# Kernel optimization log

Measured on AMD Instinct MI355X. Metric: run time of the kernel, lower is better.

The kernel has to match this reference:

```python
import jax, jax.numpy as jnp
import numpy as np

D_MODEL = 1024
NHEAD = 16
D_K = D_MODEL // NHEAD
B, S = 2, 2048
NEG_INF = float('-inf')


def setup_inputs() -> dict:
    key = jax.random.key(0)
    ks = jax.random.split(key, 12)
    sc = 1.0 / np.sqrt(D_MODEL)
    return {
        'q': jax.random.normal(ks[0], (B, S, D_MODEL), dtype=jnp.float32),
        'k': jax.random.normal(ks[1], (B, S, D_MODEL), dtype=jnp.float32),
        'q_mask': jax.random.randint(ks[2], (B, S), 0, 2, dtype=jnp.int32),
        'k_mask': jax.random.randint(ks[3], (B, S), 0, 2, dtype=jnp.int32),
        'Wq': jax.random.normal(ks[4], (D_MODEL, D_MODEL), dtype=jnp.float32) * sc,
        'bq': jnp.zeros((D_MODEL,), dtype=jnp.float32),
        'Wk': jax.random.normal(ks[5], (D_MODEL, D_MODEL), dtype=jnp.float32) * sc,
        'bk': jnp.zeros((D_MODEL,), dtype=jnp.float32),
        'Wv': jax.random.normal(ks[6], (D_MODEL, D_MODEL), dtype=jnp.float32) * sc,
        'bv': jnp.zeros((D_MODEL,), dtype=jnp.float32),
        'Wo': jax.random.normal(ks[7], (D_MODEL, D_MODEL), dtype=jnp.float32) * sc,
        'bo': jnp.zeros((D_MODEL,), dtype=jnp.float32),
        'causal_attention': 1,
    }


def _split_heads(x):  # [B,S,D] -> [B,H,S,d_k]
    b, s, _ = x.shape
    return x.reshape(b, s, NHEAD, D_K).transpose(0, 2, 1, 3)


def reference(q, k, q_mask, k_mask, Wq, bq, Wk, bk, Wv, bv, Wo, bo, causal_attention):
    v_in = k  # module uses V = K
    qh = _split_heads(q @ Wq.T + bq)
    kh = _split_heads(k @ Wk.T + bk)
    vh = _split_heads(v_in @ Wv.T + bv)
    # [B,H,Sq,Sk]
    scores = jnp.einsum('bhqd,bhkd->bhqk', qh, kh) / jnp.sqrt(jnp.float32(D_K))
    sq, sk = scores.shape[-2], scores.shape[-1]
    if causal_attention:
        causal = jnp.triu(jnp.ones((sq, sk), dtype=bool), k=1)
        scores = jnp.where(causal[None, None], NEG_INF, scores)
    scores = jnp.where(k_mask[:, None, None, :] == 0, NEG_INF, scores)
    attn = jax.nn.softmax(scores, axis=-1)
    attn = jnp.where(q_mask[:, None, :, None] == 0, 0.0, attn)
    out = jnp.einsum('bhqk,bhkd->bhqd', attn, vh)  # [B,H,Sq,d_k]
    out = out.transpose(0, 2, 1, 3).reshape(q.shape[0], sq, D_MODEL)
    return out @ Wo.T + bo
```

## Files before the change

### kernel.cpp

```cpp
#include <hip/hip_runtime.h>

typedef unsigned short u16;
typedef unsigned int   u32;
typedef __bf16 bf16x8 __attribute__((ext_vector_type(8)));
typedef float  f32x4  __attribute__((ext_vector_type(4)));

#define NEG_INF (-__builtin_inff())

#define GLDS16(g, l) __builtin_amdgcn_global_load_lds( \
    (const __attribute__((address_space(1))) void*)(g), \
    (__attribute__((address_space(3))) void*)(l), 16, 0, 0)

__device__ __forceinline__ u16 f2bf(float f) {
  u32 u = __builtin_bit_cast(u32, f);
  u32 r = u + 0x7FFFu + ((u >> 16) & 1u);
  return (u16)(r >> 16);
}
__device__ __forceinline__ float bf2f(u16 v) {
  u32 u = ((u32)v) << 16;
  return __builtin_bit_cast(float, u);
}
__device__ __forceinline__ u32 pk2bf(float a, float b) {
  return __builtin_amdgcn_perm(__builtin_bit_cast(u32, b),
                               __builtin_bit_cast(u32, a), 0x07060302u);
}
__device__ __forceinline__ float bperm(float v, int src) {
  return __builtin_bit_cast(float, __builtin_amdgcn_ds_bpermute(
      src * 4, __builtin_bit_cast(int, v)));
}

struct ConvArgs {
  const void* src[10];
  u16* dst[10];
};

__global__ void convert_kernel(ConvArgs a, const int* __restrict__ kmask,
                               float* __restrict__ kbias) {
  if (blockIdx.x >= 1024) {
    int idx = (blockIdx.x - 1024) * 256 + threadIdx.x;
    kbias[idx] = kmask[idx] ? 0.0f : NEG_INF;
    return;
  }
  __shared__ int cnt;
  if (threadIdx.x == 0) cnt = 0;
  __syncthreads();
  const u16* q16 = (const u16*)a.src[0];
  int local = 0;
  for (int i = threadIdx.x; i < 8192; i += 256) {
    int e = (q16[i] >> 7) & 0xFF;
    if (e >= 118 && e <= 129) local++;
  }
  atomicAdd(&cnt, local);
  __syncthreads();
  const int fl = (cnt > 6144) ? 1 : 0;

  const int total = 1573376;
  for (int u0 = blockIdx.x * 256 + threadIdx.x; u0 < total; u0 += 1024 * 256) {
    int s, off;
    if (u0 < 1048576)      { s = u0 >> 19;                 off = u0 & 524287; }
    else if (u0 < 1572864) { int v = u0 - 1048576; s = 2 + (v >> 17); off = v & 131071; }
    else                   { int v = u0 - 1572864; s = 6 + (v >> 7);  off = v & 127; }
    u16* d = a.dst[s] + (size_t)off * 8;
    if (fl) {
      const uint4* sp = (const uint4*)((const u16*)a.src[s] + (size_t)off * 8);
      *(uint4*)d = *sp;
    } else {
      const float* sp = (const float*)a.src[s] + (size_t)off * 8;
      u16 tmp[8];
      #pragma unroll
      for (int j = 0; j < 8; j++) tmp[j] = f2bf(sp[j]);
      *(uint4*)d = *(uint4*)tmp;
    }
  }
}

template <int BM>
__device__ __forceinline__ void gemm_mainloop(
    const u16* __restrict__ A, const u16* __restrict__ W,
    int bm, int bn, u16* As, u16* Bs, f32x4 (*acc)[4]) {
  const int t = threadIdx.x, lane = t & 63, w = t >> 6;
  const int wm = (w >> 1) * (BM / 2), wn = (w & 1) * 64;
  const int l15 = lane & 15, quad = lane >> 4;
  const int sr = t >> 2, sc = (t & 3) * 8;
  const u16* Ag0 = A + (size_t)(bm + sr) * 1024 + sc;
  const u16* Ag1 = Ag0 + (size_t)64 * 1024;
  const u16* Wg0 = W + (size_t)(bn + sr) * 1024 + sc;
  const u16* Wg1 = Wg0 + (size_t)64 * 1024;
  u16* As0 = As + t * 8;        u16* As1 = As + 2048 + t * 8;
  u16* Bs0 = Bs + t * 8;        u16* Bs1 = Bs + 2048 + t * 8;

  for (int k0 = 0; k0 < 1024; k0 += 32) {
    GLDS16(Ag0 + k0, As0);
    if (BM == 128) GLDS16(Ag1 + k0, As1);
    GLDS16(Wg0 + k0, Bs0);
    GLDS16(Wg1 + k0, Bs1);
    __syncthreads();
    bf16x8 af[BM / 32], bw[4];
    #pragma unroll
    for (int i = 0; i < BM / 32; i++)
      af[i] = *(const bf16x8*)&As[(wm + i * 16 + l15) * 32 + quad * 8];
    #pragma unroll
    for (int j = 0; j < 4; j++)
      bw[j] = *(const bf16x8*)&Bs[(wn + j * 16 + l15) * 32 + quad * 8];
    #pragma unroll
    for (int i = 0; i < BM / 32; i++)
      #pragma unroll
      for (int j = 0; j < 4; j++)
        acc[i][j] = __builtin_amdgcn_mfma_f32_16x16x32_bf16(af[i], bw[j], acc[i][j], 0, 0, 0);
    __syncthreads();
  }
}

__global__ __launch_bounds__(256) void qkv_proj_kernel(
    const u16* __restrict__ qc, const u16* __restrict__ kc,
    const u16* __restrict__ Wq, const u16* __restrict__ Wk, const u16* __restrict__ Wv,
    const u16* __restrict__ bq, const u16* __restrict__ bk, const u16* __restrict__ bv,
    u16* __restrict__ Qp, u16* __restrict__ Kp, u16* __restrict__ Vt) {
  __shared__ __align__(16) u16 As[128 * 32];
  __shared__ __align__(16) u16 Bs[128 * 32];
  const int z = blockIdx.z;
  const u16* A    = (z == 0) ? qc : kc;
  const u16* W    = (z == 0) ? Wq : (z == 1) ? Wk : Wv;
  const u16* bias = (z == 0) ? bq : (z == 1) ? bk : bv;
  const int bm = blockIdx.y * 128, bn = blockIdx.x * 128;

  const f32x4 fzero = {0.f, 0.f, 0.f, 0.f};
  f32x4 acc[4][4];
  #pragma unroll
  for (int i = 0; i < 4; i++)
    #pragma unroll
    for (int j = 0; j < 4; j++) acc[i][j] = fzero;

  gemm_mainloop<128>(A, W, bm, bn, As, Bs, acc);

  const int t = threadIdx.x, lane = t & 63, w = t >> 6;
  const int wm = (w >> 1) * 64, wn = (w & 1) * 64;
  const int l15 = lane & 15, quad = lane >> 4;

  if (z < 2) {
    u16* out = (z == 0) ? Qp : Kp;
    #pragma unroll
    for (int i = 0; i < 4; i++)
      #pragma unroll
      for (int j = 0; j < 4; j++) {
        int n = bn + wn + j * 16 + l15;
        float bb = bf2f(bias[n]);
        int m0 = bm + wm + i * 16 + quad * 4;
        #pragma unroll
        for (int r = 0; r < 4; r++)
          out[(size_t)(m0 + r) * 1024 + n] = f2bf(acc[i][j][r] + bb);
      }
  } else {
    #pragma unroll
    for (int i = 0; i < 4; i++)
      #pragma unroll
      for (int j = 0; j < 4; j++) {
        int n = bn + wn + j * 16 + l15;
        int hh = n >> 6, dw = n & 63;
        float bb = bf2f(bias[n]);
        int m0 = bm + wm + i * 16 + quad * 4;
        int b_ = m0 >> 11, s0 = m0 & 2047;
        u16 tmp[4];
        #pragma unroll
        for (int r = 0; r < 4; r++) tmp[r] = f2bf(acc[i][j][r] + bb);
        *(ushort4*)&Vt[((size_t)(b_ * 16 + hh) * 64 + dw) * 2048 + s0] = *(ushort4*)tmp;
      }
  }
}

__global__ __launch_bounds__(256, 4) void attn_kernel(
    const u16* __restrict__ Qp, const u16* __restrict__ Kp, const u16* __restrict__ Vt,
    const int* __restrict__ qmask, const float* __restrict__ kbias,
    const int* __restrict__ causal_p, u16* __restrict__ AO) {
  __shared__ __align__(16) u16 KS[2][128 * 64];
  __shared__ __align__(16) u16 VS[2][64 * 128];
  __shared__ __align__(16) u16 P[4][16 * 64];

  const int t = threadIdx.x, lane = t & 63, w = t >> 6;
  const int quad = lane >> 4, l15 = lane & 15, l7 = l15 & 7;
  const int bh = blockIdx.x & 31;
  const int g4 = 31 - (int)(blockIdx.x >> 5);
  const int b = bh >> 4, h = bh & 15;
  const int causal = *causal_p;
  const int q0 = g4 * 64 + w * 16;
  const int nkt = causal ? (g4 >> 1) + 1 : 16;
  const float cs = 0.18033688011112042f;
  const f32x4 fzero = {0.f, 0.f, 0.f, 0.f};

  const u16* qr = Qp + (size_t)(b * 2048 + q0 + l15) * 1024 + h * 64 + quad * 8;
  const bf16x8 qf0 = *(const bf16x8*)qr;
  const bf16x8 qf1 = *(const bf16x8*)(qr + 32);

  const int kLr = lane >> 3, kLc = lane & 7;
  const u16* kgw = Kp + (size_t)(b * 2048 + 32 * w + kLr) * 1024 + h * 64 +
                   (kLc ^ kLr) * 8;
  const int vLr = lane >> 4, vLc = lane & 15;
  const u16* vgw = Vt + (size_t)bh * 131072 + (size_t)(16 * w) * 2048;
  int voff[4];
  #pragma unroll
  for (int i = 0; i < 4; i++)
    voff[i] = (4 * i + vLr) * 2048 + ((vLc ^ (4 * i + vLr)) * 8);
  u16* kls0 = &KS[0][(32 * w) * 64] + lane * 8;
  u16* kls1 = &KS[1][(32 * w) * 64] + lane * 8;
  u16* vls0 = &VS[0][(16 * w) * 128] + lane * 8;
  u16* vls1 = &VS[1][(16 * w) * 128] + lane * 8;

  f32x4 Oa[4];
  #pragma unroll
  for (int dt = 0; dt < 4; dt++) Oa[dt] = fzero;
  float mr = NEG_INF, lr = 0.f;
  u16* Pw = P[w];

  {
    const u16* kg = kgw;
    const u16* vg = vgw;
    #pragma unroll
    for (int i = 0; i < 4; i++) {
      GLDS16(kg + i * 8192, kls0 + i * 512);
      GLDS16(vg + voff[i], vls0 + i * 512);
    }
  }

  for (int kt = 0; kt < nkt; kt++) {
    __syncthreads();
    if (kt + 1 < nkt) {
      const u16* kg = kgw + (size_t)(kt + 1) * 131072;
      const u16* vg = vgw + (kt + 1) * 128;
      u16* kd = ((kt + 1) & 1) ? kls1 : kls0;
      u16* vd = ((kt + 1) & 1) ? vls1 : vls0;
      #pragma unroll
      for (int i = 0; i < 4; i++) {
        GLDS16(kg + i * 8192, kd + i * 512);
        GLDS16(vg + voff[i], vd + i * 512);
      }
    }
    if (causal && kt * 128 > q0 + 15) continue;
    const u16* KSc = KS[kt & 1];
    const u16* VSc = VS[kt & 1];

    f32x4 sa[8];
    #pragma unroll
    for (int mt = 0; mt < 8; mt++) sa[mt] = fzero;
    #pragma unroll
    for (int mt = 0; mt < 8; mt++) {
      bf16x8 kf0 = *(const bf16x8*)&KSc[(mt * 16 + l15) * 64 + ((quad ^ l7) * 8)];
      bf16x8 kf1 = *(const bf16x8*)&KSc[(mt * 16 + l15) * 64 + (((quad ^ l7) ^ 4) * 8)];
      sa[mt] = __builtin_amdgcn_mfma_f32_16x16x32_bf16(kf0, qf0, sa[mt], 0, 0, 0);
      sa[mt] = __builtin_amdgcn_mfma_f32_16x16x32_bf16(kf1, qf1, sa[mt], 0, 0, 0);
    }

    const f32x4* kb4 = (const f32x4*)(kbias + b * 2048 + kt * 128);
    #pragma unroll
    for (int mt = 0; mt < 8; mt++) {
      f32x4 kb = kb4[mt * 4 + quad];
      #pragma unroll
      for (int r = 0; r < 4; r++) sa[mt][r] = sa[mt][r] * cs + kb[r];
    }
    if (causal && kt * 128 + 127 > q0) {
      #pragma unroll
      for (int mt = 0; mt < 8; mt++)
        #pragma unroll
        for (int r = 0; r < 4; r++)
          if (kt * 128 + mt * 16 + quad * 4 + r > q0 + l15) sa[mt][r] = NEG_INF;
    }

    f32x4 m4 = sa[0];
    #pragma unroll
    for (int mt = 1; mt < 8; mt++)
      #pragma unroll
      for (int r = 0; r < 4; r++) m4[r] = fmaxf(m4[r], sa[mt][r]);
    float mx = fmaxf(fmaxf(m4[0], m4[1]), fmaxf(m4[2], m4[3]));
    mx = fmaxf(mx, __shfl_xor(mx, 16, 64));
    mx = fmaxf(mx, __shfl_xor(mx, 32, 64));
    float mn = fmaxf(mr, mx);
    float mc = fmaxf(mn, -3.0e38f);
    float al = __builtin_amdgcn_exp2f(mr - mc);
    mr = mn;
    float ssum = 0.f;
    #pragma unroll
    for (int mt = 0; mt < 8; mt++)
      #pragma unroll
      for (int r = 0; r < 4; r++) {
        float pv = __builtin_amdgcn_exp2f(sa[mt][r] - mc);
        sa[mt][r] = pv;
        ssum += pv;
      }
    ssum += __shfl_xor(ssum, 16, 64);
    ssum += __shfl_xor(ssum, 32, 64);
    lr = lr * al + ssum;

    f32x4 alv;
    #pragma unroll
    for (int r = 0; r < 4; r++) alv[r] = bperm(al, quad * 4 + r);
    #pragma unroll
    for (int dt = 0; dt < 4; dt++)
      #pragma unroll
      for (int r = 0; r < 4; r++) Oa[dt][r] *= alv[r];

    #pragma unroll
    for (int hh = 0; hh < 2; hh++) {
      #pragma unroll
      for (int mh = 0; mh < 4; mh++) {
        int B = mh * 2 + (quad >> 1);
        uint2 pk;
        pk.x = pk2bf(sa[hh * 4 + mh][0], sa[hh * 4 + mh][1]);
        pk.y = pk2bf(sa[hh * 4 + mh][2], sa[hh * 4 + mh][3]);
        *(uint2*)&Pw[l15 * 64 + ((B ^ l7) * 8) + (quad & 1) * 4] = pk;
      }
      #pragma unroll
      for (int kh = 0; kh < 2; kh++) {
        int kp = hh * 2 + kh;
        bf16x8 pf = *(const bf16x8*)&Pw[l15 * 64 + (((kh * 4 + quad) ^ l7) * 8)];
        #pragma unroll
        for (int dt = 0; dt < 4; dt++) {
          bf16x8 vf = *(const bf16x8*)
              &VSc[(dt * 16 + l15) * 128 + (((kp * 4 + quad) ^ l15) * 8)];
          Oa[dt] = __builtin_amdgcn_mfma_f32_16x16x32_bf16(pf, vf, Oa[dt], 0, 0, 0);
        }
      }
    }
  }

  float f = (lr > 0.f) ? (1.0f / lr) : 0.f;
  if (qmask[b * 2048 + q0 + l15] == 0) f = 0.f;
  f32x4 fv;
  #pragma unroll
  for (int r = 0; r < 4; r++) fv[r] = bperm(f, quad * 4 + r);
  #pragma unroll
  for (int dt = 0; dt < 4; dt++)
    #pragma unroll
    for (int r = 0; r < 4; r++)
      AO[(size_t)(b * 2048 + q0 + quad * 4 + r) * 1024 + h * 64 + dt * 16 + l15] =
          f2bf(Oa[dt][r] * fv[r]);
}

__global__ __launch_bounds__(256, 2) void oproj_kernel(
    const u16* __restrict__ AO, const u16* __restrict__ Wo, const u16* __restrict__ bo,
    void* __restrict__ out, const int* __restrict__ flag) {
  __shared__ __align__(16) u16 As[64 * 32];
  __shared__ __align__(16) u16 Bs[128 * 32];
  const int bm = blockIdx.y * 64, bn = blockIdx.x * 128;

  const f32x4 fzero = {0.f, 0.f, 0.f, 0.f};
  f32x4 acc[2][4];
  #pragma unroll
  for (int i = 0; i < 2; i++)
    #pragma unroll
    for (int j = 0; j < 4; j++) acc[i][j] = fzero;

  gemm_mainloop<64>(AO, Wo, bm, bn, As, Bs, acc);

  const int t = threadIdx.x, lane = t & 63, w = t >> 6;
  const int wm = (w >> 1) * 32, wn = (w & 1) * 64;
  const int l15 = lane & 15, quad = lane >> 4;
  const int isbf = *flag;
  #pragma unroll
  for (int i = 0; i < 2; i++)
    #pragma unroll
    for (int j = 0; j < 4; j++) {
      int n = bn + wn + j * 16 + l15;
      float bb = bf2f(bo[n]);
      int m0 = bm + wm + i * 16 + quad * 4;
      #pragma unroll
      for (int r = 0; r < 4; r++) {
        float v = acc[i][j][r] + bb;
        size_t idx = (size_t)(m0 + r) * 1024 + n;
        if (isbf) ((u16*)out)[idx] = f2bf(v);
        else      ((float*)out)[idx] = v;
      }
    }
}

__global__ void flag_kernel(const u16* __restrict__ q, int* __restrict__ flag) {
  __shared__ int cnt;
  if (threadIdx.x == 0) cnt = 0;
  __syncthreads();
  int local = 0;
  for (int i = threadIdx.x; i < 8192; i += 256) {
    int e = (q[i] >> 7) & 0xFF;
    if (e >= 118 && e <= 129) local++;
  }
  atomicAdd(&cnt, local);
  __syncthreads();
  if (threadIdx.x == 0) flag[0] = (cnt > 6144) ? 1 : 0;
}

extern "C" void kernel_launch(void* const* d_in, const int* in_sizes, int n_in,
                              void* d_out, int out_size, void* d_ws, size_t ws_size,
                              hipStream_t stream) {
  (void)in_sizes; (void)n_in; (void)out_size; (void)ws_size;

  char* w = (char*)d_ws;
  int* flag = (int*)w;
  u16* qc  = (u16*)(w + 256);
  u16* kc  = qc  + 4194304;
  u16* Qp  = kc  + 4194304;
  u16* Kp  = Qp  + 4194304;
  u16* Vt  = Kp  + 4194304;
  u16* AO  = Vt  + 4194304;
  u16* Wqc = AO  + 4194304;
  u16* Wkc = Wqc + 1048576;
  u16* Wvc = Wkc + 1048576;
  u16* Woc = Wvc + 1048576;
  u16* bqc = Woc + 1048576;
  u16* bkc = bqc + 1024;
  u16* bvc = bkc + 1024;
  u16* boc = bvc + 1024;
  float* kbias = (float*)(boc + 1024);

  flag_kernel<<<1, 256, 0, stream>>>((const u16*)d_in[0], flag);

  ConvArgs ca;
  ca.src[0] = d_in[0];  ca.dst[0] = qc;
  ca.src[1] = d_in[1];  ca.dst[1] = kc;
  ca.src[2] = d_in[4];  ca.dst[2] = Wqc;
  ca.src[3] = d_in[6];  ca.dst[3] = Wkc;
  ca.src[4] = d_in[8];  ca.dst[4] = Wvc;
  ca.src[5] = d_in[10]; ca.dst[5] = Woc;
  ca.src[6] = d_in[5];  ca.dst[6] = bqc;
  ca.src[7] = d_in[7];  ca.dst[7] = bkc;
  ca.src[8] = d_in[9];  ca.dst[8] = bvc;
  ca.src[9] = d_in[11]; ca.dst[9] = boc;
  convert_kernel<<<1040, 256, 0, stream>>>(ca, (const int*)d_in[3], kbias);

  qkv_proj_kernel<<<dim3(8, 32, 3), 256, 0, stream>>>(
      qc, kc, Wqc, Wkc, Wvc, bqc, bkc, bvc, Qp, Kp, Vt);

  attn_kernel<<<1024, 256, 0, stream>>>(
      Qp, Kp, Vt, (const int*)d_in[2], kbias, (const int*)d_in[12], AO);

  oproj_kernel<<<dim3(8, 64), 256, 0, stream>>>(AO, Woc, boc, d_out, flag);
}
```

Baseline: 244.8 us.

## Double-buffer GEMM LDS tiles, swizzle block order, and fold flag kernel into convert

```diff
diff --git a/kernel.cpp b/kernel.cpp
--- a/kernel.cpp
+++ b/kernel.cpp
@@ -35,7 +35,7 @@
 };
 
 __global__ void convert_kernel(ConvArgs a, const int* __restrict__ kmask,
-                               float* __restrict__ kbias) {
+                               float* __restrict__ kbias, int* __restrict__ flag) {
   if (blockIdx.x >= 1024) {
     int idx = (blockIdx.x - 1024) * 256 + threadIdx.x;
     kbias[idx] = kmask[idx] ? 0.0f : NEG_INF;
@@ -53,6 +53,7 @@
   atomicAdd(&cnt, local);
   __syncthreads();
   const int fl = (cnt > 6144) ? 1 : 0;
+  if (blockIdx.x == 0 && threadIdx.x == 0) flag[0] = fl;
 
   const int total = 1573376;
   for (int u0 = blockIdx.x * 256 + threadIdx.x; u0 < total; u0 += 1024 * 256) {
@@ -77,7 +78,7 @@
 template <int BM>
 __device__ __forceinline__ void gemm_mainloop(
     const u16* __restrict__ A, const u16* __restrict__ W,
-    int bm, int bn, u16* As, u16* Bs, f32x4 (*acc)[4]) {
+    int bm, int bn, u16 (*As)[BM * 32], u16 (*Bs)[128 * 32], f32x4 (*acc)[4]) {
   const int t = threadIdx.x, lane = t & 63, w = t >> 6;
   const int wm = (w >> 1) * (BM / 2), wn = (w & 1) * 64;
   const int l15 = lane & 15, quad = lane >> 4;
@@ -86,28 +87,33 @@
   const u16* Ag1 = Ag0 + (size_t)64 * 1024;
   const u16* Wg0 = W + (size_t)(bn + sr) * 1024 + sc;
   const u16* Wg1 = Wg0 + (size_t)64 * 1024;
-  u16* As0 = As + t * 8;        u16* As1 = As + 2048 + t * 8;
-  u16* Bs0 = Bs + t * 8;        u16* Bs1 = Bs + 2048 + t * 8;
-
-  for (int k0 = 0; k0 < 1024; k0 += 32) {
-    GLDS16(Ag0 + k0, As0);
-    if (BM == 128) GLDS16(Ag1 + k0, As1);
-    GLDS16(Wg0 + k0, Bs0);
-    GLDS16(Wg1 + k0, Bs1);
+
+  GLDS16(Ag0, As[0] + t * 8);
+  if (BM == 128) GLDS16(Ag1, As[0] + 2048 + t * 8);
+  GLDS16(Wg0, Bs[0] + t * 8);
+  GLDS16(Wg1, Bs[0] + 2048 + t * 8);
+
+  int st = 0;
+  for (int k0 = 0; k0 < 1024; k0 += 32, st ^= 1) {
     __syncthreads();
+    if (k0 + 32 < 1024) {
+      GLDS16(Ag0 + k0 + 32, As[st ^ 1] + t * 8);
+      if (BM == 128) GLDS16(Ag1 + k0 + 32, As[st ^ 1] + 2048 + t * 8);
+      GLDS16(Wg0 + k0 + 32, Bs[st ^ 1] + t * 8);
+      GLDS16(Wg1 + k0 + 32, Bs[st ^ 1] + 2048 + t * 8);
+    }
     bf16x8 af[BM / 32], bw[4];
     #pragma unroll
     for (int i = 0; i < BM / 32; i++)
-      af[i] = *(const bf16x8*)&As[(wm + i * 16 + l15) * 32 + quad * 8];
+      af[i] = *(const bf16x8*)&As[st][(wm + i * 16 + l15) * 32 + quad * 8];
     #pragma unroll
     for (int j = 0; j < 4; j++)
-      bw[j] = *(const bf16x8*)&Bs[(wn + j * 16 + l15) * 32 + quad * 8];
+      bw[j] = *(const bf16x8*)&Bs[st][(wn + j * 16 + l15) * 32 + quad * 8];
     #pragma unroll
     for (int i = 0; i < BM / 32; i++)
       #pragma unroll
       for (int j = 0; j < 4; j++)
         acc[i][j] = __builtin_amdgcn_mfma_f32_16x16x32_bf16(af[i], bw[j], acc[i][j], 0, 0, 0);
-    __syncthreads();
   }
 }
 
@@ -116,13 +122,16 @@
     const u16* __restrict__ Wq, const u16* __restrict__ Wk, const u16* __restrict__ Wv,
     const u16* __restrict__ bq, const u16* __restrict__ bk, const u16* __restrict__ bv,
     u16* __restrict__ Qp, u16* __restrict__ Kp, u16* __restrict__ Vt) {
-  __shared__ __align__(16) u16 As[128 * 32];
-  __shared__ __align__(16) u16 Bs[128 * 32];
-  const int z = blockIdx.z;
+  __shared__ __align__(16) u16 As[2][128 * 32];
+  __shared__ __align__(16) u16 Bs[2][128 * 32];
+  const int bid = blockIdx.x;
+  const int g = ((bid >> 6) << 3) | (bid & 7);
+  const int xb = (bid >> 3) & 7;
+  const int yb = g & 31, z = g >> 5;
   const u16* A    = (z == 0) ? qc : kc;
   const u16* W    = (z == 0) ? Wq : (z == 1) ? Wk : Wv;
   const u16* bias = (z == 0) ? bq : (z == 1) ? bk : bv;
-  const int bm = blockIdx.y * 128, bn = blockIdx.x * 128;
+  const int bm = yb * 128, bn = xb * 128;
 
   const f32x4 fzero = {0.f, 0.f, 0.f, 0.f};
   f32x4 acc[4][4];
@@ -337,9 +346,12 @@
 __global__ __launch_bounds__(256, 2) void oproj_kernel(
     const u16* __restrict__ AO, const u16* __restrict__ Wo, const u16* __restrict__ bo,
     void* __restrict__ out, const int* __restrict__ flag) {
-  __shared__ __align__(16) u16 As[64 * 32];
-  __shared__ __align__(16) u16 Bs[128 * 32];
-  const int bm = blockIdx.y * 64, bn = blockIdx.x * 128;
+  __shared__ __align__(16) u16 As[2][64 * 32];
+  __shared__ __align__(16) u16 Bs[2][128 * 32];
+  const int bid = blockIdx.x;
+  const int g = ((bid >> 6) << 3) | (bid & 7);
+  const int xb = (bid >> 3) & 7;
+  const int bm = g * 64, bn = xb * 128;
 
   const f32x4 fzero = {0.f, 0.f, 0.f, 0.f};
   f32x4 acc[2][4];
@@ -369,20 +381,6 @@
         else      ((float*)out)[idx] = v;
       }
     }
-}
-
-__global__ void flag_kernel(const u16* __restrict__ q, int* __restrict__ flag) {
-  __shared__ int cnt;
-  if (threadIdx.x == 0) cnt = 0;
-  __syncthreads();
-  int local = 0;
-  for (int i = threadIdx.x; i < 8192; i += 256) {
-    int e = (q[i] >> 7) & 0xFF;
-    if (e >= 118 && e <= 129) local++;
-  }
-  atomicAdd(&cnt, local);
-  __syncthreads();
-  if (threadIdx.x == 0) flag[0] = (cnt > 6144) ? 1 : 0;
 }
 
 extern "C" void kernel_launch(void* const* d_in, const int* in_sizes, int n_in,
@@ -408,8 +406,6 @@
   u16* boc = bvc + 1024;
   float* kbias = (float*)(boc + 1024);
 
-  flag_kernel<<<1, 256, 0, stream>>>((const u16*)d_in[0], flag);
-
   ConvArgs ca;
   ca.src[0] = d_in[0];  ca.dst[0] = qc;
   ca.src[1] = d_in[1];  ca.dst[1] = kc;
@@ -421,13 +417,13 @@
   ca.src[7] = d_in[7];  ca.dst[7] = bkc;
   ca.src[8] = d_in[9];  ca.dst[8] = bvc;
   ca.src[9] = d_in[11]; ca.dst[9] = boc;
-  convert_kernel<<<1040, 256, 0, stream>>>(ca, (const int*)d_in[3], kbias);
-
-  qkv_proj_kernel<<<dim3(8, 32, 3), 256, 0, stream>>>(
+  convert_kernel<<<1040, 256, 0, stream>>>(ca, (const int*)d_in[3], kbias, flag);
+
+  qkv_proj_kernel<<<768, 256, 0, stream>>>(
       qc, kc, Wqc, Wkc, Wvc, bqc, bkc, bvc, Qp, Kp, Vt);
 
   attn_kernel<<<1024, 256, 0, stream>>>(
       Qp, Kp, Vt, (const int*)d_in[2], kbias, (const int*)d_in[12], AO);
 
-  oproj_kernel<<<dim3(8, 64), 256, 0, stream>>>(AO, Woc, boc, d_out, flag);
-}
+  oproj_kernel<<<512, 256, 0, stream>>>(AO, Woc, boc, d_out, flag);
+}
```

After: 243.4 us. No clear change (-0.6%).
